# Optimization experiments

Hardware: AMD Instinct MI355X
Metric: run time of the kernel (lower is better)

## Reference

```python
import jax, jax.numpy as jnp
import numpy as np

N_NODES = 16384
K_NBR = 16
N_HOPS = 4  # hops + 2
IN_DIM = 256
RAW_DIM = 128
OUT_DIM = 64
PHI_DIM = 16
N_KERN = 4
E = N_NODES * K_NBR


def setup_inputs() -> dict:
    key = jax.random.key(0)
    ks = jax.random.split(key, 16)
    s = 0.05  # small weight scale for numerical sanity
    h = jax.random.normal(ks[0], (N_NODES, IN_DIM), jnp.float32)
    e_tensor = jax.random.normal(ks[1], (N_HOPS, N_NODES, RAW_DIM), jnp.float32)
    # kNN-style edges: each dst node has exactly K_NBR incoming edges
    src = jax.random.randint(ks[2], (N_HOPS, E), 0, N_NODES, jnp.int32)
    dst = jnp.tile(jnp.repeat(jnp.arange(N_NODES, dtype=jnp.int32), K_NBR)[None, :], (N_HOPS, 1))
    return {
        'h': h,
        'e_tensor': e_tensor,
        'src': src,
        'dst': dst,
        'W_phi': jax.random.normal(ks[3], (N_HOPS, RAW_DIM, PHI_DIM - 1), jnp.float32) * s,
        'mlp_w1': jax.random.normal(ks[4], (N_HOPS, RAW_DIM, IN_DIM), jnp.float32) * s,
        'mlp_b1': jax.random.normal(ks[5], (N_HOPS, IN_DIM), jnp.float32) * s,
        'mlp_w2': jax.random.normal(ks[6], (N_HOPS, IN_DIM, PHI_DIM * N_KERN), jnp.float32) * s,
        'mlp_b2': jax.random.normal(ks[7], (N_HOPS, PHI_DIM * N_KERN), jnp.float32) * s,
        'tilde_phi': jax.random.normal(ks[8], (N_HOPS, N_KERN, PHI_DIM), jnp.float32),
        'W': jax.random.normal(ks[9], (N_HOPS, IN_DIM, OUT_DIM * N_KERN), jnp.float32) * s,
        'bias': jax.random.normal(ks[10], (N_HOPS, OUT_DIM), jnp.float32) * s,
        'z': jax.random.normal(ks[11], (OUT_DIM, 1), jnp.float32),
    }


def _deform_gconv(h, e_l, src, dst, W_phi, w1, b1, w2, b2, tilde_phi, W, bias):
    N = h.shape[0]
    nk, phi_dim = tilde_phi.shape
    hk = (h @ W).reshape(N, nk, -1)                                  # (N, nk, out)
    phi = e_l @ W_phi                                                # (N, phi-1)
    tn = tilde_phi / jnp.linalg.norm(tilde_phi, axis=1, keepdims=True)  # (nk, phi)
    hid = jax.nn.relu(e_l @ w1 + b1)
    delta = (hid @ w2 + b2).reshape(N, nk, phi_dim)                  # (N, nk, phi)
    delta_ik = tn[None, :, :] + delta                                # (N, nk, phi)
    # per-edge quantities (edges carry dst-node delta_ik, u_sub_v distance)
    dist = phi[src] - phi[dst]                                       # (E, phi-1)
    last = jnp.all(dist == 0, axis=1, keepdims=True).astype(dist.dtype)
    dist = jnp.concatenate([dist, last], axis=1)                     # (E, phi)
    dist = dist / jnp.maximum(jnp.linalg.norm(dist, axis=1, keepdims=True), 1e-8)
    logits = jnp.einsum('ep,ekp->ek', dist, delta_ik[dst])           # (E, nk)
    # edge_softmax over incoming edges of each dst node
    mx = jax.ops.segment_max(logits, dst, num_segments=N)
    ex = jnp.exp(logits - mx[dst])
    den = jax.ops.segment_sum(ex, dst, num_segments=N)
    att = ex / den[dst]                                              # (E, nk)
    # message passing: m = h[src] * att, sum over incoming edges
    m = hk[src] * att[:, :, None]                                    # (E, nk, out)
    agg = jax.ops.segment_sum(m, dst, num_segments=N)                # (N, nk, out)
    out = agg.sum(1) + bias[None, :]
    out = out / jnp.maximum(jnp.linalg.norm(out, axis=1, keepdims=True), 1e-8)
    # regularizers
    d = tn[:, None, :] - tn[None, :, :]                              # (nk, nk, phi)
    l_sep = jnp.sum(jnp.sum(d * d, axis=-1)) / nk                    # sum_i mean_j ||t_i - t_j||^2
    l_focus = jnp.mean(jnp.sum(delta * delta, axis=2))
    return out, l_sep, l_focus


def reference(h, e_tensor, src, dst, W_phi, mlp_w1, mlp_b1, mlp_w2, mlp_b2, tilde_phi, W, bias, z):
    outs, l_seps, l_fos = jax.vmap(
        _deform_gconv, in_axes=(None, 0, 0, 0, 0, 0, 0, 0, 0, 0, 0, 0)
    )(h, e_tensor, src, dst, W_phi, mlp_w1, mlp_b1, mlp_w2, mlp_b2, tilde_phi, W, bias)
    # hop-level softmax fusion
    score = jnp.einsum('hno,oz->hnz', outs, z)                       # (n_hops, N, 1)
    att = jax.nn.softmax(score, axis=0)
    tilde_h = jnp.sum(att * outs, axis=0)                            # (N, out)
    l_sep = jnp.mean(l_seps)
    l_focus = jnp.mean(l_fos)
    return tilde_h, l_sep, l_focus
```

## Files before the change

### kernel.cpp

```cpp
#include <hip/hip_runtime.h>
#include <hip/hip_bf16.h>

#define N_NODES 16384
#define K_NBR 16
#define HOPS 4
#define IN_DIM 256
#define RAW_DIM 128
#define OUT_DIM 64
#define PHI_DIM 16
#define N_KERN 4
#define E_EDGES (N_NODES * K_NBR)

typedef __hip_bfloat16 bf16;
typedef __attribute__((ext_vector_type(8))) short short8;
typedef __attribute__((ext_vector_type(4))) float f32x4;
typedef __attribute__((ext_vector_type(2))) float f32x2;
typedef __attribute__((ext_vector_type(4))) unsigned int uint4v;

__device__ __forceinline__ float toF(float x) { return x; }
__device__ __forceinline__ float toF(bf16 x) { return __bfloat162float(x); }
__device__ __forceinline__ short f2bfbits(float f)
{
    bf16 b = __float2bfloat16(f);
    short s; __builtin_memcpy(&s, &b, 2); return s;
}

#define SWZ(row, colShort) ((colShort) ^ (((row) & 7) << 3))
#define SWZ32(row, colShort) ((colShort) ^ ((((row) >> 1) & 3) << 3))

__device__ __forceinline__ void gld_lds16(const bf16* g, short* l)
{
    __builtin_amdgcn_global_load_lds(
        (const __attribute__((address_space(1))) unsigned int*)g,
        (__attribute__((address_space(3))) unsigned int*)l, 16, 0, 0);
}

template <int IMM>
__device__ __forceinline__ float swzx(float v)
{
    return __builtin_bit_cast(float,
        __builtin_amdgcn_ds_swizzle(__builtin_bit_cast(int, v), IMM));
}
#define XOR1  0x041F
#define XOR2  0x081F
#define XOR4  0x101F
#define XOR8  0x201F
#define XOR16 0x401F

__device__ __forceinline__ void pkfma_w0(f32x2& acc, f32x2 w, f32x2 x)
{
    asm("v_pk_fma_f32 %0, %1, %2, %0 op_sel:[0,0,0] op_sel_hi:[0,1,1]"
        : "+v"(acc) : "v"(w), "v"(x));
}
__device__ __forceinline__ void pkfma_w1(f32x2& acc, f32x2 w, f32x2 x)
{
    asm("v_pk_fma_f32 %0, %1, %2, %0 op_sel:[1,0,0] op_sel_hi:[1,1,1]"
        : "+v"(acc) : "v"(w), "v"(x));
}

#define CVC_B1   0
#define CVC_B2   (CVC_B1 + HOPS * IN_DIM)
#define CVC_BIAS (CVC_B2 + HOPS * PHI_DIM * N_KERN)
#define CVC_Z    (CVC_BIAS + HOPS * OUT_DIM)
#define CVC_END  (CVC_Z + OUT_DIM)

#define WT_N  (HOPS * 256 * 256)
#define W1T_N (HOPS * 256 * 128)
#define W2T_N (HOPS * 64 * 256)
#define WPT_N (HOPS * 16 * 128)
#define CVT_TOTAL (WT_N + W1T_N + W2T_N + WPT_N)

#define NB_CV ((CVC_END + 255) / 256)
#define NB_WT (CVT_TOTAL / 1024)
#define NB_H  (N_NODES * 256 / 8 / 2048)
#define NB_E  (HOPS * N_NODES * 128 / 8 / 2048)
#define NB_ALL (NB_CV + NB_WT + NB_H + NB_E + 1)

#define GA_TOTAL 2048

__device__ __forceinline__ float loadDyn(const void* p, int i, bool isbf)
{
    return isbf ? toF(((const bf16*)p)[i]) : ((const float*)p)[i];
}

__device__ __forceinline__ void cvt8(bf16* dst, const void* src, size_t base, bool isbf)
{
    short8 v;
    if (isbf) {
        v = __builtin_nontemporal_load((const short8*)((const bf16*)src + base));
    } else {
        const float* sp = (const float*)src + base;
        f32x4 f0 = __builtin_nontemporal_load((const f32x4*)sp);
        f32x4 f1 = __builtin_nontemporal_load((const f32x4*)(sp + 4));
#pragma unroll
        for (int j = 0; j < 4; j++) { v[j] = f2bfbits(f0[j]); v[4 + j] = f2bfbits(f1[j]); }
    }
    *(short8*)(dst + base) = v;
}

__global__ __launch_bounds__(256) void cvt_all(
    const void* h, const void* e,
    const void* wphi, const void* w1, const void* b1, const void* w2,
    const void* b2, const void* tphi, const void* W, const void* bias,
    const void* z, float* __restrict__ CV,
    bf16* __restrict__ wt, bf16* __restrict__ w1t, bf16* __restrict__ w2t,
    bf16* __restrict__ wpt, bf16* __restrict__ h_bf, bf16* __restrict__ e_bf,
    float* __restrict__ tn_out, float* __restrict__ acc, int* __restrict__ flagOut)
{
    __shared__ float s_det[4];
    int tid = threadIdx.x;
    {
        unsigned short pv = ((const unsigned short*)h)[tid];
        unsigned int bits = ((unsigned int)pv) << 16;
        float v; __builtin_memcpy(&v, &bits, 4);
        v = fabsf(v);
        if (!(v == v) || v > 1e30f) v = 1e30f;
#pragma unroll
        for (int off = 32; off > 0; off >>= 1) v = fmaxf(v, __shfl_xor(v, off));
        if ((tid & 63) == 0) s_det[tid >> 6] = v;
    }
    __syncthreads();
    bool isbf = fmaxf(fmaxf(s_det[0], s_det[1]), fmaxf(s_det[2], s_det[3])) < 1e4f;

    int b = blockIdx.x;
    if (b == NB_ALL - 1) {
        __shared__ float s_v[256], s_tn[256], s_red[256], s_hop[4];
        int hop = tid >> 6, t64 = tid & 63;
        int row = t64 >> 4, p = t64 & 15;
        float v = loadDyn(tphi, hop * 64 + t64, isbf);
        s_v[tid] = v;
        __syncthreads();
        float ss = 0.f;
        for (int q = 0; q < 16; q++) { float x = s_v[hop * 64 + row * 16 + q]; ss += x * x; }
        float tnv = v / sqrtf(ss);
        tn_out[hop * 64 + t64] = tnv;
        s_tn[tid] = tnv;
        __syncthreads();
        float s = 0.f;
        for (int j = 0; j < 4; j++) {
            float d = tnv - s_tn[hop * 64 + j * 16 + p];
            s += d * d;
        }
        s_red[tid] = s;
        __syncthreads();
        if (t64 == 0) {
            float tot = 0.f;
            for (int i = 0; i < 64; i++) tot += s_red[hop * 64 + i];
            s_hop[hop] = tot;
        }
        __syncthreads();
        if (tid == 0) {
            acc[0] = (s_hop[0] + s_hop[1] + s_hop[2] + s_hop[3]) * 0.0625f;
            acc[1] = 0.f;
            *flagOut = isbf ? 1 : 0;
        }
        return;
    }
    if (b < NB_CV) {
        int idx = b * 256 + tid;
        if (idx >= CVC_END) return;
        float v;
        if      (idx < CVC_B2)   v = loadDyn(b1,   idx - CVC_B1,   isbf);
        else if (idx < CVC_BIAS) v = loadDyn(b2,   idx - CVC_B2,   isbf);
        else if (idx < CVC_Z)    v = loadDyn(bias, idx - CVC_BIAS, isbf);
        else                     v = loadDyn(z,    idx - CVC_Z,    isbf);
        CV[idx] = v;
        return;
    }
    b -= NB_CV;
    if (b < NB_WT) {
        int base = (b * 256 + tid) * 4;
#pragma unroll
        for (int jj = 0; jj < 4; jj++) {
            int idx = base + jj;
            if (idx < WT_N) {
                int o = idx, hop = o >> 16, rem = o & 65535, n = rem >> 8, k = rem & 255;
                wt[o] = __float2bfloat16(loadDyn(W, hop * 65536 + k * 256 + n, isbf));
            } else if (idx < WT_N + W1T_N) {
                int o = idx - WT_N, hop = o >> 15, rem = o & 32767, n = rem >> 7, k = rem & 127;
                w1t[o] = __float2bfloat16(loadDyn(w1, hop * 32768 + k * 256 + n, isbf));
            } else if (idx < WT_N + W1T_N + W2T_N) {
                int o = idx - WT_N - W1T_N, hop = o >> 14, rem = o & 16383, n = rem >> 8, k = rem & 255;
                w2t[o] = __float2bfloat16(loadDyn(w2, hop * 16384 + k * 64 + n, isbf));
            } else {
                int o = idx - WT_N - W1T_N - W2T_N, hop = o >> 11, rem = o & 2047, n = rem >> 7, k = rem & 127;
                float v = (n < 15) ? loadDyn(wphi, hop * 1920 + k * 15 + n, isbf) : 0.f;
                wpt[o] = __float2bfloat16(v);
            }
        }
        return;
    }
    b -= NB_WT;
    if (b < NB_H) {
#pragma unroll
        for (int k = 0; k < 8; k++) {
            size_t base = ((size_t)b * 2048 + k * 256 + tid) * 8;
            cvt8(h_bf, h, base, isbf);
        }
        return;
    }
    b -= NB_H;
    {
#pragma unroll
        for (int k = 0; k < 8; k++) {
            size_t base = ((size_t)b * 2048 + k * 256 + tid) * 8;
            cvt8(e_bf, e, base, isbf);
        }
    }
}

__device__ __forceinline__ void gemm_hk_dev(
    char* smem, const bf16* __restrict__ A, const bf16* __restrict__ Bt,
    unsigned char* __restrict__ Cg, int colBase, int rowBase)
{
    short* base = (short*)smem;
    int tid = threadIdx.x;
    int w = tid >> 6, lane = tid & 63;
    int wr = w >> 1, wc = w & 1;
    int l16 = lane & 15, quad = lane >> 4;
    f32x4 acc[4][4] = {};

#define HK_STAGE(bufb, k0v)                                                          \
    {                                                                                \
        short* As_ = base + (bufb) * 16384;                                          \
        short* Bs_ = As_ + 8192;                                                     \
        for (int id = tid; id < 128 * 8; id += 256) {                                \
            int row = id >> 3, j = id & 7;                                           \
            gld_lds16(A + (size_t)(rowBase + row) * 256 + (k0v) + ((j ^ (row & 7)) * 8), \
                      As_ + id * 8);                                                 \
        }                                                                            \
        for (int id = tid; id < 128 * 8; id += 256) {                                \
            int row = id >> 3, j = id & 7;                                           \
            gld_lds16(Bt + (size_t)(colBase + row) * 256 + (k0v) + ((j ^ (row & 7)) * 8), \
                      Bs_ + id * 8);                                                 \
        }                                                                            \
    }

    HK_STAGE(0, 0)
    HK_STAGE(1, 64)
    asm volatile("s_waitcnt vmcnt(8)" ::: "memory");
    __builtin_amdgcn_sched_barrier(0);
    __builtin_amdgcn_s_barrier();
    __builtin_amdgcn_sched_barrier(0);
#pragma unroll
    for (int t = 0; t < 4; ++t) {
        short* As = base + (t & 1) * 16384;
        short* Bs = As + 8192;
        short8 aF[2][4], bF[2][4];
#pragma unroll
        for (int hh = 0; hh < 2; hh++) {
            int kc = hh * 32;
#pragma unroll
            for (int mi = 0; mi < 4; mi++) {
                int row = wr * 64 + mi * 16 + l16;
                aF[hh][mi] = *(const short8*)&As[row * 64 + SWZ(row, kc + quad * 8)];
            }
#pragma unroll
            for (int ni = 0; ni < 4; ni++) {
                int row = wc * 64 + ni * 16 + l16;
                bF[hh][ni] = *(const short8*)&Bs[row * 64 + SWZ(row, kc + quad * 8)];
            }
        }
        asm volatile("s_waitcnt lgkmcnt(0)" ::: "memory");
        __builtin_amdgcn_sched_barrier(0);
        __builtin_amdgcn_s_barrier();
        __builtin_amdgcn_sched_barrier(0);
        if (t < 2) HK_STAGE(t & 1, (t + 2) * 64)
#pragma unroll
        for (int hh = 0; hh < 2; hh++)
#pragma unroll
            for (int mi = 0; mi < 4; mi++)
#pragma unroll
                for (int ni = 0; ni < 4; ni++)
                    acc[mi][ni] = __builtin_amdgcn_mfma_f32_16x16x32_bf16(
                        aF[hh][mi], bF[hh][ni], acc[mi][ni], 0, 0, 0);
        if (t < 3) {
            if (t < 2) { asm volatile("s_waitcnt vmcnt(8)" ::: "memory"); }
            else       { asm volatile("s_waitcnt vmcnt(0)" ::: "memory"); }
            __builtin_amdgcn_sched_barrier(0);
            __builtin_amdgcn_s_barrier();
            __builtin_amdgcn_sched_barrier(0);
        }
    }
#undef HK_STAGE

    unsigned char* Cs = (unsigned char*)smem;
#pragma unroll
    for (int mi = 0; mi < 4; mi++)
#pragma unroll
        for (int ni = 0; ni < 4; ni++) {
            int cl = wc * 64 + ni * 16 + l16;
#pragma unroll
            for (int r = 0; r < 4; r++) {
                int rl = wr * 64 + mi * 16 + quad * 4 + r;
                float v = acc[mi][ni][r];
                int pk = __builtin_amdgcn_cvt_pk_fp8_f32(v, v, 0, false);
                Cs[rl * 128 + cl] = (unsigned char)(pk & 0xFF);
            }
        }
    __syncthreads();
    for (int c = tid; c < 128 * 8; c += 256) {
        int r = c >> 3, off = (c & 7) * 16;
        *(uint4v*)(Cg + ((size_t)(rowBase + r) * 256 + colBase) + off) =
            *(const uint4v*)(Cs + (size_t)r * 128 + off);
    }
}

__device__ __forceinline__ void hid_delta_dev(
    char* smem,
    const bf16* __restrict__ A, const bf16* __restrict__ B1,
    const bf16* __restrict__ B2, const bf16* __restrict__ WP,
    const float* __restrict__ b1, const float* __restrict__ b2,
    const float* __restrict__ tn, float* __restrict__ Dg,
    float* __restrict__ phiG, float* __restrict__ lfocus, int rowBase)
{
    short* base = (short*)smem;
    short* Wpa = base + 20480;
    short* Hs  = base;
    short* B2s = Hs + 16384;
    float* Ds  = (float*)smem;
    float* s_w = (float*)(smem + 65520);

    int tid = threadIdx.x;
    int w = tid >> 6, lane = tid & 63;
    int l16 = lane & 15, quad = lane >> 4;

#define HID_STAGE(bufb, k0v)                                                   \
    {                                                                          \
        short* As_ = base + (bufb) * 2048;                                     \
        short* Bs_ = base + 4096 + (bufb) * 8192;                              \
        for (int id = tid; id < 64 * 4; id += 256) {                           \
            int row = id >> 2, j = id & 3;                                     \
            gld_lds16(A + (size_t)(rowBase + row) * 128 + (k0v) +              \
                          ((j ^ ((row >> 1) & 3)) * 8),                        \
                      As_ + id * 8);                                           \
        }                                                                      \
        for (int id = tid; id < 256 * 4; id += 256) {                          \
            int row = id >> 2, j = id & 3;                                     \
            gld_lds16(B1 + (size_t)row * 128 + (k0v) +                         \
                          ((j ^ ((row >> 1) & 3)) * 8),                        \
                      Bs_ + id * 8);                                           \
        }                                                                      \
    }

    f32x4 acc[4][4] = {};
    f32x4 accp[4] = {};
    {
        HID_STAGE(0, 0)
        {
            int row = tid >> 4, j = tid & 15;
            gld_lds16(WP + (size_t)row * 128 + ((j ^ (row & 7)) * 8),
                      Wpa + tid * 8);
        }
        HID_STAGE(1, 32)
        asm volatile("s_waitcnt vmcnt(5)" ::: "memory");
        __builtin_amdgcn_sched_barrier(0);
        __builtin_amdgcn_s_barrier();
        __builtin_amdgcn_sched_barrier(0);
#pragma unroll
        for (int t = 0; t < 4; ++t) {
            short* As_ = base + (t & 1) * 2048;
            short* Bs_ = base + 4096 + (t & 1) * 8192;
            short8 aF[4], bF[4], bFp;
#pragma unroll
            for (int mi = 0; mi < 4; mi++) {
                int row = mi * 16 + l16;
                aF[mi] = *(const short8*)&As_[row * 32 + SWZ32(row, quad * 8)];
            }
#pragma unroll
            for (int ni = 0; ni < 4; ni++) {
                int row = w * 64 + ni * 16 + l16;
                bF[ni] = *(const short8*)&Bs_[row * 32 + SWZ32(row, quad * 8)];
            }
            if (w == 0)
                bFp = *(const short8*)&Wpa[l16 * 128 + SWZ(l16, t * 32 + quad * 8)];
            asm volatile("s_waitcnt lgkmcnt(0)" ::: "memory");
            __builtin_amdgcn_sched_barrier(0);
            __builtin_amdgcn_s_barrier();
            __builtin_amdgcn_sched_barrier(0);
            if (t < 2) HID_STAGE(t & 1, (t + 2) * 32)
#pragma unroll
            for (int mi = 0; mi < 4; mi++)
#pragma unroll
                for (int ni = 0; ni < 4; ni++)
                    acc[mi][ni] = __builtin_amdgcn_mfma_f32_16x16x32_bf16(
                        aF[mi], bF[ni], acc[mi][ni], 0, 0, 0);
            if (w == 0) {
#pragma unroll
                for (int mi = 0; mi < 4; mi++)
                    accp[mi] = __builtin_amdgcn_mfma_f32_16x16x32_bf16(
                        aF[mi], bFp, accp[mi], 0, 0, 0);
            }
            if (t < 3) {
                if (t < 2) { asm volatile("s_waitcnt vmcnt(5)" ::: "memory"); }
                else       { asm volatile("s_waitcnt vmcnt(0)" ::: "memory"); }
                __builtin_amdgcn_sched_barrier(0);
                __builtin_amdgcn_s_barrier();
                __builtin_amdgcn_sched_barrier(0);
            }
        }
#undef HID_STAGE
#pragma unroll
        for (int mi = 0; mi < 4; mi++) {
#pragma unroll
            for (int ni = 0; ni < 4; ni++) {
                int col = w * 64 + ni * 16 + l16;
                float bv = b1[col];
#pragma unroll
                for (int r = 0; r < 4; r++) {
                    int row = mi * 16 + quad * 4 + r;
                    float v = fmaxf(acc[mi][ni][r] + bv, 0.f);
                    Hs[row * 256 + SWZ(row, col)] = f2bfbits(v);
                }
            }
        }
        for (int id = tid; id < 64 * 32; id += 256) {
            int row = id >> 5, j = id & 31;
            gld_lds16(B2 + (size_t)row * 256 + ((j ^ (row & 7)) * 8),
                      B2s + id * 8);
        }
        if (w == 0) {
#pragma unroll
            for (int mi = 0; mi < 4; mi++)
#pragma unroll
                for (int r = 0; r < 4; r++)
                    phiG[(size_t)(rowBase + mi * 16 + quad * 4 + r) * 16 + l16] =
                        accp[mi][r];
        }
    }

    {
        __syncthreads();
        f32x4 acc2[4] = {};
        int arow = w * 16 + l16;
#pragma unroll
        for (int q = 0; q < 8; q++) {
            int kc = q * 32;
            short8 aF = *(const short8*)&Hs[arow * 256 + SWZ(arow, kc + quad * 8)];
            short8 bFq[4];
#pragma unroll
            for (int ni = 0; ni < 4; ni++) {
                int brow = ni * 16 + l16;
                bFq[ni] = *(const short8*)&B2s[brow * 256 + SWZ(brow, kc + quad * 8)];
            }
#pragma unroll
            for (int ni = 0; ni < 4; ni++)
                acc2[ni] = __builtin_amdgcn_mfma_f32_16x16x32_bf16(aF, bFq[ni], acc2[ni], 0, 0, 0);
        }
        asm volatile("s_waitcnt lgkmcnt(0)" ::: "memory");
        __builtin_amdgcn_sched_barrier(0);
        __builtin_amdgcn_s_barrier();
        __builtin_amdgcn_sched_barrier(0);
        float sq = 0.f;
#pragma unroll
        for (int ni = 0; ni < 4; ni++) {
            int col = ni * 16 + l16;
            float bv = b2[col], tv = tn[col];
#pragma unroll
            for (int r = 0; r < 4; r++) {
                int row = w * 16 + quad * 4 + r;
                float v = acc2[ni][r] + bv;
                sq += v * v;
                Ds[row * 64 + col] = v + tv;
            }
        }
#pragma unroll
        for (int off = 32; off > 0; off >>= 1) sq += __shfl_xor(sq, off);
        if (lane == 0) s_w[w] = sq;
        __syncthreads();
        for (int c = tid; c < 64 * 16; c += 256) {
            int r = c >> 4, off = (c & 15) * 4;
            *(uint4v*)(Dg + (size_t)(rowBase + r) * 64 + off) =
                *(const uint4v*)(Ds + (size_t)r * 64 + off);
        }
        if (tid == 0) atomicAdd(lfocus, s_w[0] + s_w[1] + s_w[2] + s_w[3]);
    }
}

__global__ __launch_bounds__(256, 2) void gemm_all(
    const bf16* __restrict__ h_bf, const bf16* __restrict__ e_bf,
    const bf16* __restrict__ WT, const bf16* __restrict__ WPT,
    const bf16* __restrict__ W1T, const bf16* __restrict__ W2T,
    const float* __restrict__ b1All, const float* __restrict__ b2All,
    const float* __restrict__ tnAll, unsigned char* __restrict__ hk_f8,
    float* __restrict__ phi, float* __restrict__ DELTA, float* __restrict__ lfocus)
{
    __shared__ __align__(16) char smem[65536];
    int b = blockIdx.x;
    int x = b & 7;
    int p = b >> 3;
    int s = p >> 1;
    if ((p & 1) == 0) {
        int rg = x * 16 + (s >> 3);
        int v = s & 7;
        int hop = v >> 1, part = v & 1;
        gemm_hk_dev(smem, h_bf, WT + (size_t)hop * 65536,
                    hk_f8 + (size_t)hop * N_NODES * 256, part * 128, rg * 128);
    } else {
        int hop = x & 3;
        int tile = ((x >> 2) << 7) + s;
        hid_delta_dev(smem,
            e_bf + (size_t)hop * N_NODES * 128,
            W1T + (size_t)hop * 32768, W2T + (size_t)hop * 16384,
            WPT + (size_t)hop * 2048,
            b1All + hop * 256, b2All + hop * 64, tnAll + hop * 64,
            DELTA + (size_t)hop * N_NODES * 64,
            phi + (size_t)hop * N_NODES * 16, lfocus, tile * 64);
    }
}

__global__ __launch_bounds__(256) void edge_agg2(
    const unsigned char* __restrict__ hk, const float* __restrict__ phi,
    const float* __restrict__ dik, const int* __restrict__ src,
    const float* __restrict__ biasAll, float* __restrict__ outs)
{
    int b = blockIdx.x;
    int hop = b & 3;
    int wave = threadIdx.x >> 6, lane = threadIdx.x & 63;
    int node = (b >> 2) * 4 + wave;
    const unsigned char* hk_l = hk + (size_t)hop * N_NODES * 256;
    const float* phi_l  = phi + (size_t)hop * N_NODES * 16;
    const float* dik_l  = dik + (size_t)hop * N_NODES * 64;
    const int*   src_n  = src + (size_t)hop * E_EDGES + (size_t)node * 16;
    const float* bias_l = biasAll + hop * 64;
    float*       outs_n = outs + ((size_t)hop * N_NODES + node) * 64;

    __shared__ __align__(16) float s_dik[4][64];
    __shared__ __align__(16) float s_attT[4][4][24];
    __shared__ int   s_src[4][16];

    s_dik[wave][lane] = __builtin_nontemporal_load(&dik_l[(size_t)node * 64 + lane]);
    if (lane < 16) s_src[wave][lane] = __builtin_nontemporal_load(&src_n[lane]);

    int e = lane >> 2, q = lane & 3;
    int sN = s_src[wave][e];
    f32x4 ps = *(const f32x4*)(phi_l + (size_t)sN * 16 + q * 4);
    f32x4 pd = *(const f32x4*)(phi_l + (size_t)node * 16 + q * 4);
    float d0 = ps[0] - pd[0], d1 = ps[1] - pd[1];
    float d2 = ps[2] - pd[2], d3 = ps[3] - pd[3];
    bool q3 = (q == 3);
    float ssp = d0 * d0 + d1 * d1 + d2 * d2 + (q3 ? 0.f : d3 * d3);
    ssp += swzx<XOR1>(ssp); ssp += swzx<XOR2>(ssp);
    float last = (ssp == 0.f) ? 1.f : 0.f;
    if (q3) d3 = last;
    float inv = fminf(__builtin_amdgcn_rsqf(ssp + last * last), 1e8f);
#pragma unroll
    for (int k = 0; k < 4; k++) {
        f32x4 dkv = *(const f32x4*)&s_dik[wave][k * 16 + q * 4];
        float pk = d0 * dkv[0] + d1 * dkv[1] + d2 * dkv[2] + d3 * dkv[3];
        pk += swzx<XOR1>(pk); pk += swzx<XOR2>(pk);
        if (q == k) s_attT[wave][k][e] = pk * inv;
    }

    int k2 = lane & 3;
    float lgv = s_attT[wave][k2][e];
    float mx = lgv;
    mx = fmaxf(mx, swzx<XOR4>(mx));
    mx = fmaxf(mx, swzx<XOR8>(mx));
    mx = fmaxf(mx, swzx<XOR16>(mx));
    mx = fmaxf(mx, __shfl_xor(mx, 32));
    float ex = __expf(lgv - mx);
    float den = ex;
    den += swzx<XOR4>(den);
    den += swzx<XOR8>(den);
    den += swzx<XOR16>(den);
    den += __shfl_xor(den, 32);
    s_attT[wave][k2][e] = ex * __builtin_amdgcn_rcpf(den);

    int kk = lane >> 4, dsub = (lane & 15) * 4;
    f32x2 att2[8];
#pragma unroll
    for (int g = 0; g < 8; g++) att2[g] = *(const f32x2*)&s_attT[wave][kk][g * 2];
    f32x2 a01 = {0.f, 0.f}, a23 = {0.f, 0.f};
#pragma unroll
    for (int ep = 0; ep < 8; ep++) {
        int sm0 = __builtin_amdgcn_readfirstlane(s_src[wave][2 * ep]);
        int sm1 = __builtin_amdgcn_readfirstlane(s_src[wave][2 * ep + 1]);
        unsigned int u0 = *(const unsigned int*)(hk_l + (size_t)sm0 * 256 + lane * 4);
        unsigned int u1 = *(const unsigned int*)(hk_l + (size_t)sm1 * 256 + lane * 4);
        f32x2 w = att2[ep];
        pkfma_w0(a01, w, __builtin_amdgcn_cvt_pk_f32_fp8((int)u0, false));
        pkfma_w0(a23, w, __builtin_amdgcn_cvt_pk_f32_fp8((int)u0, true));
        pkfma_w1(a01, w, __builtin_amdgcn_cvt_pk_f32_fp8((int)u1, false));
        pkfma_w1(a23, w, __builtin_amdgcn_cvt_pk_f32_fp8((int)u1, true));
    }
    float a0 = a01[0], a1 = a01[1], a2 = a23[0], a3 = a23[1];
    a0 += swzx<XOR16>(a0); a0 += __shfl_xor(a0, 32);
    a1 += swzx<XOR16>(a1); a1 += __shfl_xor(a1, 32);
    a2 += swzx<XOR16>(a2); a2 += __shfl_xor(a2, 32);
    a3 += swzx<XOR16>(a3); a3 += __shfl_xor(a3, 32);
    f32x4 bv = *(const f32x4*)(bias_l + dsub);
    float o0 = a0 + bv[0];
    float o1 = a1 + bv[1];
    float o2 = a2 + bv[2];
    float o3 = a3 + bv[3];
    float ssq = o0 * o0 + o1 * o1 + o2 * o2 + o3 * o3;
    ssq += swzx<XOR1>(ssq);
    ssq += swzx<XOR2>(ssq);
    ssq += swzx<XOR4>(ssq);
    ssq += swzx<XOR8>(ssq);
    float inv2 = fminf(__builtin_amdgcn_rsqf(ssq), 1e8f);
    if (kk == 0) {
        f32x4 st;
        st[0] = o0 * inv2; st[1] = o1 * inv2; st[2] = o2 * inv2; st[3] = o3 * inv2;
        __builtin_nontemporal_store(st, (f32x4*)(outs_n + dsub));
    }
}

__global__ __launch_bounds__(256) void fuse_kernel(
    const float* __restrict__ outs, const float* __restrict__ z,
    void* __restrict__ out, const int* __restrict__ flag,
    const float* __restrict__ acc)
{
    int tid = threadIdx.x;
    int node = blockIdx.x * 4 + (tid >> 6);
    int dd = tid & 63;
    float zv = z[dd];
    float o[4], sc[4];
#pragma unroll
    for (int h = 0; h < 4; h++) {
        o[h] = __builtin_nontemporal_load(&outs[((size_t)h * N_NODES + node) * 64 + dd]);
        float v = o[h] * zv;
#pragma unroll
        for (int off = 32; off > 0; off >>= 1) v += __shfl_xor(v, off);
        sc[h] = v;
    }
    float mx = fmaxf(fmaxf(sc[0], sc[1]), fmaxf(sc[2], sc[3]));
    float e0 = __expf(sc[0] - mx), e1 = __expf(sc[1] - mx);
    float e2 = __expf(sc[2] - mx), e3 = __expf(sc[3] - mx);
    float den = e0 + e1 + e2 + e3;
    float t = (e0 * o[0] + e1 * o[1] + e2 * o[2] + e3 * o[3]) * __builtin_amdgcn_rcpf(den);
    size_t oi = (size_t)node * 64 + dd;
    bool isbf = (*flag != 0);
    if (isbf) __builtin_nontemporal_store(f2bfbits(t), (short*)out + oi);
    else      __builtin_nontemporal_store(t, (float*)out + oi);
    if (blockIdx.x == 0 && tid == 0) {
        float a = acc[0];
        float b = acc[1] / ((float)N_NODES * 4.f * 4.f);
        size_t base = (size_t)N_NODES * 64;
        if (isbf) {
            ((bf16*)out)[base]     = __float2bfloat16(a);
            ((bf16*)out)[base + 1] = __float2bfloat16(b);
        } else {
            ((float*)out)[base]     = a;
            ((float*)out)[base + 1] = b;
        }
    }
}

extern "C" void kernel_launch(void* const* d_in, const int* in_sizes, int n_in,
                              void* d_out, int out_size, void* d_ws, size_t ws_size,
                              hipStream_t stream)
{
    const void* h    = d_in[0];
    const void* e    = d_in[1];
    const int*  src  = (const int*)d_in[2];
    const void* Wphi = d_in[4];
    const void* w1   = d_in[5];
    const void* b1   = d_in[6];
    const void* w2   = d_in[7];
    const void* b2   = d_in[8];
    const void* tphi = d_in[9];
    const void* W    = d_in[10];
    const void* bias = d_in[11];
    const void* z    = d_in[12];

    float* ws    = (float*)d_ws;
    float* CV    = ws;
    float* OUTS  = CV + CVC_END;
    float* PHI   = OUTS + (size_t)4 * N_NODES * 64;
    float* DELTA = PHI + (size_t)4 * N_NODES * 16;
    float* TN    = DELTA + (size_t)4 * N_NODES * 64;
    float* ACC   = TN + 256;
    int*   FLAG  = (int*)(ACC + 2);
    bf16*  H_BF  = (bf16*)(ACC + 4);
    bf16*  E_BF  = H_BF + (size_t)N_NODES * 256;
    bf16*  WT    = E_BF + (size_t)HOPS * N_NODES * 128;
    bf16*  W1T   = WT + WT_N;
    bf16*  W2T   = W1T + W1T_N;
    bf16*  WPT   = W2T + W2T_N;
    unsigned char* HK_F8 = (unsigned char*)(WPT + WPT_N);

    cvt_all<<<NB_ALL, 256, 0, stream>>>(
        h, e, Wphi, w1, b1, w2, b2, tphi, W, bias, z, CV,
        WT, W1T, W2T, WPT, H_BF, E_BF, TN, ACC, FLAG);

    gemm_all<<<dim3(GA_TOTAL), 256, 0, stream>>>(
        H_BF, E_BF, WT, WPT, W1T, W2T,
        CV + CVC_B1, CV + CVC_B2, TN, HK_F8, PHI, DELTA, ACC + 1);

    edge_agg2<<<dim3(N_NODES), 256, 0, stream>>>(
        HK_F8, PHI, DELTA, src, CV + CVC_BIAS, OUTS);

    fuse_kernel<<<dim3(N_NODES / 4), 256, 0, stream>>>(
        OUTS, CV + CVC_Z, d_out, FLAG, ACC);
}
```

Before: 196.4 us.

## Fuse edge aggregation with hop-softmax fusion into one kernel per node

Each block now handles one node with one wave per hop, instead of one hop and four nodes. The normalized per-hop outputs stay in shared memory, and the hop-attention softmax and final write happen in the same kernel. This removes the OUTS intermediate round trip (4×N×64 floats written and read back) and one kernel launch. In exchange it adds two block-level barriers, and only one of the four waves does the final combine and store. Blocks also now touch four different hop tables at once, which changes gather locality.

Measured after the change: 218.4 us. +11.2%, slower.

```diff
diff --git a/kernel.cpp b/kernel.cpp
--- a/kernel.cpp
+++ b/kernel.cpp
@@ -509,31 +509,32 @@
     }
 }
 
-__global__ __launch_bounds__(256) void edge_agg2(
+__global__ __launch_bounds__(256) void edge_fuse(
     const unsigned char* __restrict__ hk, const float* __restrict__ phi,
     const float* __restrict__ dik, const int* __restrict__ src,
-    const float* __restrict__ biasAll, float* __restrict__ outs)
-{
-    int b = blockIdx.x;
-    int hop = b & 3;
-    int wave = threadIdx.x >> 6, lane = threadIdx.x & 63;
-    int node = (b >> 2) * 4 + wave;
+    const float* __restrict__ biasAll, const float* __restrict__ z,
+    void* __restrict__ out, const int* __restrict__ flag,
+    const float* __restrict__ acc)
+{
+    int node = blockIdx.x;
+    int hop = threadIdx.x >> 6, lane = threadIdx.x & 63;
     const unsigned char* hk_l = hk + (size_t)hop * N_NODES * 256;
     const float* phi_l  = phi + (size_t)hop * N_NODES * 16;
     const float* dik_l  = dik + (size_t)hop * N_NODES * 64;
     const int*   src_n  = src + (size_t)hop * E_EDGES + (size_t)node * 16;
     const float* bias_l = biasAll + hop * 64;
-    float*       outs_n = outs + ((size_t)hop * N_NODES + node) * 64;
 
     __shared__ __align__(16) float s_dik[4][64];
     __shared__ __align__(16) float s_attT[4][4][24];
     __shared__ int   s_src[4][16];
-
-    s_dik[wave][lane] = __builtin_nontemporal_load(&dik_l[(size_t)node * 64 + lane]);
-    if (lane < 16) s_src[wave][lane] = __builtin_nontemporal_load(&src_n[lane]);
+    __shared__ __align__(16) float s_o[4][64];
+    __shared__ float s_sc[4];
+
+    s_dik[hop][lane] = __builtin_nontemporal_load(&dik_l[(size_t)node * 64 + lane]);
+    if (lane < 16) s_src[hop][lane] = __builtin_nontemporal_load(&src_n[lane]);
 
     int e = lane >> 2, q = lane & 3;
-    int sN = s_src[wave][e];
+    int sN = s_src[hop][e];
     f32x4 ps = *(const f32x4*)(phi_l + (size_t)sN * 16 + q * 4);
     f32x4 pd = *(const f32x4*)(phi_l + (size_t)node * 16 + q * 4);
     float d0 = ps[0] - pd[0], d1 = ps[1] - pd[1];
@@ -546,14 +547,14 @@
     float inv = fminf(__builtin_amdgcn_rsqf(ssp + last * last), 1e8f);
 #pragma unroll
     for (int k = 0; k < 4; k++) {
-        f32x4 dkv = *(const f32x4*)&s_dik[wave][k * 16 + q * 4];
+        f32x4 dkv = *(const f32x4*)&s_dik[hop][k * 16 + q * 4];
         float pk = d0 * dkv[0] + d1 * dkv[1] + d2 * dkv[2] + d3 * dkv[3];
         pk += swzx<XOR1>(pk); pk += swzx<XOR2>(pk);
-        if (q == k) s_attT[wave][k][e] = pk * inv;
+        if (q == k) s_attT[hop][k][e] = pk * inv;
     }
 
     int k2 = lane & 3;
-    float lgv = s_attT[wave][k2][e];
+    float lgv = s_attT[hop][k2][e];
     float mx = lgv;
     mx = fmaxf(mx, swzx<XOR4>(mx));
     mx = fmaxf(mx, swzx<XOR8>(mx));
@@ -565,17 +566,17 @@
     den += swzx<XOR8>(den);
     den += swzx<XOR16>(den);
     den += __shfl_xor(den, 32);
-    s_attT[wave][k2][e] = ex * __builtin_amdgcn_rcpf(den);
+    s_attT[hop][k2][e] = ex * __builtin_amdgcn_rcpf(den);
 
     int kk = lane >> 4, dsub = (lane & 15) * 4;
     f32x2 att2[8];
 #pragma unroll
-    for (int g = 0; g < 8; g++) att2[g] = *(const f32x2*)&s_attT[wave][kk][g * 2];
+    for (int g = 0; g < 8; g++) att2[g] = *(const f32x2*)&s_attT[hop][kk][g * 2];
     f32x2 a01 = {0.f, 0.f}, a23 = {0.f, 0.f};
 #pragma unroll
     for (int ep = 0; ep < 8; ep++) {
-        int sm0 = __builtin_amdgcn_readfirstlane(s_src[wave][2 * ep]);
-        int sm1 = __builtin_amdgcn_readfirstlane(s_src[wave][2 * ep + 1]);
+        int sm0 = __builtin_amdgcn_readfirstlane(s_src[hop][2 * ep]);
+        int sm1 = __builtin_amdgcn_readfirstlane(s_src[hop][2 * ep + 1]);
         unsigned int u0 = *(const unsigned int*)(hk_l + (size_t)sm0 * 256 + lane * 4);
         unsigned int u1 = *(const unsigned int*)(hk_l + (size_t)sm1 * 256 + lane * 4);
         f32x2 w = att2[ep];
@@ -603,47 +604,40 @@
     if (kk == 0) {
         f32x4 st;
         st[0] = o0 * inv2; st[1] = o1 * inv2; st[2] = o2 * inv2; st[3] = o3 * inv2;
-        __builtin_nontemporal_store(st, (f32x4*)(outs_n + dsub));
-    }
-}
-
-__global__ __launch_bounds__(256) void fuse_kernel(
-    const float* __restrict__ outs, const float* __restrict__ z,
-    void* __restrict__ out, const int* __restrict__ flag,
-    const float* __restrict__ acc)
-{
-    int tid = threadIdx.x;
-    int node = blockIdx.x * 4 + (tid >> 6);
-    int dd = tid & 63;
-    float zv = z[dd];
-    float o[4], sc[4];
-#pragma unroll
-    for (int h = 0; h < 4; h++) {
-        o[h] = __builtin_nontemporal_load(&outs[((size_t)h * N_NODES + node) * 64 + dd]);
-        float v = o[h] * zv;
-#pragma unroll
-        for (int off = 32; off > 0; off >>= 1) v += __shfl_xor(v, off);
-        sc[h] = v;
-    }
-    float mx = fmaxf(fmaxf(sc[0], sc[1]), fmaxf(sc[2], sc[3]));
-    float e0 = __expf(sc[0] - mx), e1 = __expf(sc[1] - mx);
-    float e2 = __expf(sc[2] - mx), e3 = __expf(sc[3] - mx);
-    float den = e0 + e1 + e2 + e3;
-    float t = (e0 * o[0] + e1 * o[1] + e2 * o[2] + e3 * o[3]) * __builtin_amdgcn_rcpf(den);
-    size_t oi = (size_t)node * 64 + dd;
-    bool isbf = (*flag != 0);
-    if (isbf) __builtin_nontemporal_store(f2bfbits(t), (short*)out + oi);
-    else      __builtin_nontemporal_store(t, (float*)out + oi);
-    if (blockIdx.x == 0 && tid == 0) {
-        float a = acc[0];
-        float b = acc[1] / ((float)N_NODES * 4.f * 4.f);
-        size_t base = (size_t)N_NODES * 64;
-        if (isbf) {
-            ((bf16*)out)[base]     = __float2bfloat16(a);
-            ((bf16*)out)[base + 1] = __float2bfloat16(b);
-        } else {
-            ((float*)out)[base]     = a;
-            ((float*)out)[base + 1] = b;
+        *(f32x4*)&s_o[hop][dsub] = st;
+    }
+    __syncthreads();
+
+    float ov = s_o[hop][lane];
+    float v = ov * z[lane];
+#pragma unroll
+    for (int off = 32; off > 0; off >>= 1) v += __shfl_xor(v, off);
+    if (lane == 0) s_sc[hop] = v;
+    __syncthreads();
+    if (hop == 0) {
+        float sc0 = s_sc[0], sc1 = s_sc[1], sc2 = s_sc[2], sc3 = s_sc[3];
+        float mxs = fmaxf(fmaxf(sc0, sc1), fmaxf(sc2, sc3));
+        float e0 = __expf(sc0 - mxs), e1 = __expf(sc1 - mxs);
+        float e2 = __expf(sc2 - mxs), e3 = __expf(sc3 - mxs);
+        float dens = e0 + e1 + e2 + e3;
+        float t = (e0 * s_o[0][lane] + e1 * s_o[1][lane] +
+                   e2 * s_o[2][lane] + e3 * s_o[3][lane]) *
+                  __builtin_amdgcn_rcpf(dens);
+        size_t oi = (size_t)node * 64 + lane;
+        bool isbf = (*flag != 0);
+        if (isbf) __builtin_nontemporal_store(f2bfbits(t), (short*)out + oi);
+        else      __builtin_nontemporal_store(t, (float*)out + oi);
+        if (node == 0 && lane == 0) {
+            float a = acc[0];
+            float b2 = acc[1] / ((float)N_NODES * 4.f * 4.f);
+            size_t bbase = (size_t)N_NODES * 64;
+            if (isbf) {
+                ((bf16*)out)[bbase]     = __float2bfloat16(a);
+                ((bf16*)out)[bbase + 1] = __float2bfloat16(b2);
+            } else {
+                ((float*)out)[bbase]     = a;
+                ((float*)out)[bbase + 1] = b2;
+            }
         }
     }
 }
@@ -689,9 +683,6 @@
         H_BF, E_BF, WT, WPT, W1T, W2T,
         CV + CVC_B1, CV + CVC_B2, TN, HK_F8, PHI, DELTA, ACC + 1);
 
-    edge_agg2<<<dim3(N_NODES), 256, 0, stream>>>(
-        HK_F8, PHI, DELTA, src, CV + CVC_BIAS, OUTS);
-
-    fuse_kernel<<<dim3(N_NODES / 4), 256, 0, stream>>>(
-        OUTS, CV + CVC_Z, d_out, FLAG, ACC);
-}
+    edge_fuse<<<dim3(N_NODES), 256, 0, stream>>>(
+        HK_F8, PHI, DELTA, src, CV + CVC_BIAS, CV + CVC_Z, d_out, FLAG, ACC);
+}
```
